# Performance work log

Measured on AMD Instinct MI355X. Metric: run time of the kernel, lower is better.

Reference implementation:

```python
import jax, jax.numpy as jnp
import numpy as np

D_MODEL = 1024
NUM_HEADS = 16
HEAD_DIM = D_MODEL // NUM_HEADS  # 64
ROPE_THETA = 10000.0
SEQ_LEN = 4096
BATCH = 1


def apply_rope(x, positions, theta=ROPE_THETA):
    # x: [b, h, s, d], positions: [s]
    d = x.shape[-1]
    inv_freq = theta ** (-jnp.arange(0, d, 2, dtype=jnp.float32) / d)  # [d/2]
    angles = positions.astype(jnp.float32)[:, None] * inv_freq[None, :]  # [s, d/2]
    cos = jnp.cos(angles)  # [s, d/2]
    sin = jnp.sin(angles)
    x1 = x[..., 0::2]  # [b, h, s, d/2]
    x2 = x[..., 1::2]
    r1 = x1 * cos - x2 * sin
    r2 = x1 * sin + x2 * cos
    # interleave back to [..., d]
    out = jnp.stack([r1, r2], axis=-1).reshape(x.shape)
    return out.astype(x.dtype)


def setup_inputs() -> dict:
    key = jax.random.key(0)
    k_x, k_qkv, k_o = jax.random.split(key, 3)
    scale_in = 1.0 / np.sqrt(D_MODEL)
    return {
        "x": jax.random.normal(k_x, (BATCH, SEQ_LEN, D_MODEL), dtype=jnp.float32),
        "token_positions": jnp.arange(SEQ_LEN, dtype=jnp.int64 if jax.config.jax_enable_x64 else jnp.int32),
        "w_qkv": jax.random.normal(k_qkv, (3 * D_MODEL, D_MODEL), dtype=jnp.float32) * scale_in,
        "w_o": jax.random.normal(k_o, (D_MODEL, D_MODEL), dtype=jnp.float32) * scale_in,
    }


def reference(x, token_positions, w_qkv, w_o):
    b, s, _ = x.shape
    # QKV projection (Linear without bias, weight [out, in])
    x_qkv = jnp.einsum('bsd,ed->bse', x, w_qkv)  # [b, s, 3*d_model]
    # rearrange 'b s (three heads kv) -> three b heads s kv'
    x_qkv = x_qkv.reshape(b, s, 3, NUM_HEADS, HEAD_DIM)
    x_qkv = jnp.transpose(x_qkv, (2, 0, 3, 1, 4))  # [3, b, h, s, d]
    q, k, v = x_qkv[0], x_qkv[1], x_qkv[2]
    q = apply_rope(q, token_positions)
    k = apply_rope(k, token_positions)
    # scaled dot-product attention with causal mask
    scores = jnp.einsum('bhnd,bhmd->bhnm', q, k) / jnp.sqrt(jnp.float32(HEAD_DIM))
    causal = jnp.tril(jnp.ones((s, s), dtype=bool))  # [s, s]
    scores = jnp.where(causal[None, None], scores, jnp.float32(-jnp.inf))
    weights = jax.nn.softmax(scores, axis=-1)
    attn = jnp.einsum('bhnm,bhmd->bhnd', weights, v)  # [b, h, s, d]
    attn = jnp.transpose(attn, (0, 2, 1, 3)).reshape(b, s, NUM_HEADS * HEAD_DIM)
    return jnp.einsum('bsd,ed->bse', attn, w_o)
```

## Files before the change

### kernel.cpp

```cpp
#include <hip/hip_runtime.h>

#define SEQ 4096
#define DMODEL 1024
#define HEADS 16
#define HD 64
#define NQKV 3072

typedef __attribute__((ext_vector_type(8))) __bf16 bf16x8;
typedef __attribute__((ext_vector_type(4))) __bf16 bf16x4;
typedef __attribute__((ext_vector_type(8))) short short8;
typedef __attribute__((ext_vector_type(4))) float f32x4;
typedef __attribute__((ext_vector_type(16))) float f32x16;
typedef __attribute__((ext_vector_type(4))) unsigned int u32x4;

__device__ __forceinline__ unsigned short f2bf(float f) {
    unsigned u = __builtin_bit_cast(unsigned, f);
    return (unsigned short)((u + 0x7fffu + ((u >> 16) & 1u)) >> 16);
}
__device__ __forceinline__ float bf2f(unsigned short h) {
    return __builtin_bit_cast(float, (unsigned)h << 16);
}
__device__ __forceinline__ unsigned cvt_pk_bf16(float lo, float hi) {
    unsigned r;
    asm("v_cvt_pk_bf16_f32 %0, %1, %2" : "=v"(r) : "v"(lo), "v"(hi));
    return r;
}

__device__ __forceinline__ void gload16(const void* g, void* l) {
    __builtin_amdgcn_global_load_lds(
        (const __attribute__((address_space(1))) unsigned int*)g,
        (__attribute__((address_space(3))) unsigned int*)l, 16, 0, 0);
}

#define TS(qt, kh) (0x40 | ((kh) << 5) | (qt))
__device__ __constant__ unsigned char TASKS[28] = {
    TS(15,0), TS(15,1), TS(14,0), TS(14,1), TS(13,0), TS(13,1),
    TS(12,0), TS(12,1), TS(11,0), TS(11,1), TS(10,0), TS(10,1),
    TS(9,0),  TS(9,1),  TS(8,0),  TS(8,1),  TS(7,0),  TS(7,1),
    3,        TS(6,0),  TS(6,1),  2,        TS(5,0),  TS(5,1),
    TS(4,0),  TS(4,1),  1,        0
};

__global__ void f2bf_all(const float* __restrict__ x, const float* __restrict__ wqkv,
                         const float* __restrict__ wo, const int* __restrict__ pos,
                         unsigned short* __restrict__ dst,
                         float* __restrict__ csT, float* __restrict__ snT) {
    const int N0 = SEQ * DMODEL / 4;
    const int N1 = N0 + NQKV * DMODEL / 4;
    const int NT = N1 + DMODEL * DMODEL / 4;
    int i = blockIdx.x * 256 + threadIdx.x;
    int stride = gridDim.x * 256;
    for (; i < NT; i += stride) {
        const float4* src;
        if (i < N0)      src = reinterpret_cast<const float4*>(x) + i;
        else if (i < N1) src = reinterpret_cast<const float4*>(wqkv) + (i - N0);
        else             src = reinterpret_cast<const float4*>(wo) + (i - N1);
        float4 f = *src;
        ushort4 o;
        o.x = f2bf(f.x); o.y = f2bf(f.y); o.z = f2bf(f.z); o.w = f2bf(f.w);
        reinterpret_cast<ushort4*>(dst)[i] = o;
    }
    const float kk = -13.287712379549449f / 32.0f;
    for (int idx = blockIdx.x * 256 + threadIdx.x; idx < SEQ * 32; idx += stride) {
        int s = idx >> 5, fi = idx & 31;
        float p = (float)pos[s];
        float ang = p * exp2f((float)fi * kk);
        float sn_, cs_;
        sincosf(ang, &sn_, &cs_);
        csT[idx] = cs_;
        snT[idx] = sn_;
    }
}

template <int EPI>
__global__ __launch_bounds__(256) void gemm_bt(const unsigned short* __restrict__ A,
                                               const unsigned short* __restrict__ B,
                                               float* __restrict__ outF,
                                               unsigned short* __restrict__ outB,
                                               unsigned short* __restrict__ vtp,
                                               const float* __restrict__ csT,
                                               const float* __restrict__ snT,
                                               int M, int N, int K) {
    alignas(16) __shared__ unsigned short a_lds[2][128 * 32];
    alignas(16) __shared__ unsigned short b_lds[2][128 * 32];
    __shared__ unsigned short vtile[4][16][72];
    const int tid = threadIdx.x;
    const int wave = tid >> 6, lane = tid & 63;
    const int l16 = lane & 15, g = lane >> 4;
    const int wr = wave >> 1, wc = wave & 1;
    const int bm = blockIdx.x, bn = blockIdx.y;

    const int lrow = lane >> 2;
    const int lcol = (lane & 3) * 8;

    const unsigned short* Ag = A + (size_t)(bm * 128 + lrow) * K + lcol;
    const unsigned short* Bg = B + (size_t)(bn * 128 + lrow) * K + lcol;

    f32x4 acc[4][4] = {};
    const int NS = K / 32;

    auto STAGE = [&](int b, int ks) {
#pragma unroll
        for (int j = 0; j < 2; ++j) {
            int chunk = wave * 2 + j;
            gload16(Ag + (size_t)(chunk * 16) * K + ks * 32, a_lds[b] + chunk * 512);
            gload16(Bg + (size_t)(chunk * 16) * K + ks * 32, b_lds[b] + chunk * 512);
        }
    };

    STAGE(0, 0);

    for (int ks = 0; ks < NS; ++ks) {
        const int cur = ks & 1;
        asm volatile("s_waitcnt vmcnt(0)" ::: "memory");
        __builtin_amdgcn_s_barrier();
        if (ks + 1 < NS) STAGE(cur ^ 1, ks + 1);

        bf16x8 af[4], bfr[4];
#pragma unroll
        for (int m = 0; m < 4; ++m)
            af[m] = *reinterpret_cast<const bf16x8*>(a_lds[cur] + (wr * 64 + m * 16 + l16) * 32 + g * 8);
#pragma unroll
        for (int n = 0; n < 4; ++n)
            bfr[n] = *reinterpret_cast<const bf16x8*>(b_lds[cur] + (wc * 64 + n * 16 + l16) * 32 + g * 8);
        __builtin_amdgcn_s_setprio(1);
#pragma unroll
        for (int m = 0; m < 4; ++m)
#pragma unroll
            for (int n = 0; n < 4; ++n)
                acc[m][n] = __builtin_amdgcn_mfma_f32_16x16x32_bf16(af[m], bfr[n], acc[m][n], 0, 0, 0);
        __builtin_amdgcn_s_setprio(0);
    }

    if (EPI == 0) {
        const float QS = 0.125f * 1.4426950408889634f;
#pragma unroll
        for (int n = 0; n < 4; ++n) {
            const int col = bn * 128 + wc * 64 + n * 16 + l16;
            const int part = col >> 10;
            const int hh = (col >> 6) & 15;
            const int d = n * 16 + l16;
            if (part < 2) {
                const int fi = (col & 63) >> 1;
                const float sc = (part == 0) ? QS : 1.0f;
                const bool odd = (col & 1) != 0;
#pragma unroll
                for (int m = 0; m < 4; ++m)
#pragma unroll
                    for (int r = 0; r < 4; ++r) {
                        int row = bm * 128 + wr * 64 + m * 16 + g * 4 + r;
                        float v = acc[m][n][r];
                        float pp = __shfl_xor(v, 1);
                        float cs_ = csT[row * 32 + fi];
                        float sn_ = snT[row * 32 + fi];
                        float out = odd ? (pp * sn_ + v * cs_) : (v * cs_ - pp * sn_);
                        outB[(size_t)((part * HEADS + hh) * SEQ + row) * HD + (col & 63)] = f2bf(out * sc);
                    }
            } else {
#pragma unroll
                for (int m = 0; m < 4; ++m)
#pragma unroll
                    for (int r = 0; r < 4; ++r)
                        vtile[wave][l16][m * 16 + g * 4 + r] = f2bf(acc[m][n][r]);
#pragma unroll
                for (int dd = 0; dd < 16; ++dd) {
                    int dg = ((col & 63) & ~15) + dd;
                    vtp[(size_t)(hh * HD + dg) * SEQ + bm * 128 + wr * 64 + lane] =
                        vtile[wave][dd][lane];
                }
            }
        }
    } else {
#pragma unroll
        for (int m = 0; m < 4; ++m)
#pragma unroll
            for (int n = 0; n < 4; ++n)
#pragma unroll
                for (int r = 0; r < 4; ++r) {
                    int row = bm * 128 + wr * 64 + m * 16 + g * 4 + r;
                    int col = bn * 128 + wc * 64 + n * 16 + l16;
                    outF[(size_t)row * N + col] = acc[m][n][r];
                }
    }
}

__global__ __launch_bounds__(512) void attn_kernel(const unsigned short* __restrict__ qkv,
                                                   const unsigned short* __restrict__ vt,
                                                   unsigned short* __restrict__ attnout,
                                                   int* __restrict__ qcnt,
                                                   unsigned short* __restrict__ pO,
                                                   float* __restrict__ lmf) {
    const int xcd = blockIdx.x & 7;
    const int tid = threadIdx.x;
    const int wave = tid >> 6, lane = tid & 63;
    const int l32 = lane & 31, hi = lane >> 5;

    alignas(16) __shared__ unsigned short k_lds[2][128 * 64];
    alignas(16) __shared__ unsigned short v_lds[2][2][64 * 64];
    __shared__ int slot_sh;

    const int rsw = (l32 & 7) << 4;

    for (;;) {
        if (tid == 0) slot_sh = atomicAdd(&qcnt[xcd], 1);
        __syncthreads();
        const int t = slot_sh;
        __syncthreads();
        if (t >= 56) break;

        const int hloc = t & 1;
        const unsigned char e = TASKS[t >> 1];
        const int qtile = e & 31;
        const int khalf = (e >> 5) & 1;
        const bool isSplit = (e >> 6) != 0;
        const int T = 2 * qtile + 2, Hh = qtile + 1;
        const int k0 = isSplit ? (khalf ? Hh : 0) : 0;
        const int k1 = isSplit ? (khalf ? T : Hh) : T;
        const int h = xcd * 2 + hloc;

        const unsigned short* Qg = qkv + (size_t)((0 * HEADS + h) * SEQ) * HD;
        const unsigned short* Kg = qkv + (size_t)((1 * HEADS + h) * SEQ) * HD;
        const unsigned short* VTg = vt + (size_t)h * HD * SEQ;

        const int qbase = qtile * 256 + wave * 32;
        const int qrow = qbase + l32;

        bf16x8 qf[4];
#pragma unroll
        for (int dg = 0; dg < 4; ++dg)
            qf[dg] = *reinterpret_cast<const bf16x8*>(Qg + (size_t)qrow * HD + dg * 16 + hi * 8);

        f32x16 oa[2] = {};
        float m_r = -1e30f, l_r = 0.f;

        auto STAGE = [&](int b, int kt) {
#pragma unroll
            for (int i = 0; i < 2; ++i) {
                int base = wave * 2048 + i * 1024;
                int byte = base + lane * 16;
                int krow = byte >> 7;
                int kc8 = ((byte >> 4) & 7) ^ (krow & 7);
                gload16(Kg + (size_t)(kt * 128 + krow) * HD + kc8 * 8, (char*)k_lds[b] + base);
                int fr = byte >> 7;
                int h64 = fr >> 6, vd = fr & 63;
                int vc8 = ((byte >> 4) & 7) ^ (vd & 7);
                gload16(VTg + (size_t)vd * SEQ + kt * 128 + h64 * 64 + vc8 * 8,
                        (char*)v_lds[b] + base);
            }
        };

        STAGE(0, k0);

        for (int kt = k0; kt < k1; ++kt) {
            const int cur = (kt - k0) & 1;
            asm volatile("s_waitcnt vmcnt(0)" ::: "memory");
            __builtin_amdgcn_s_barrier();
            if (kt + 1 < k1) STAGE(cur ^ 1, kt + 1);

#pragma unroll
            for (int hh = 0; hh < 2; ++hh) {
                if (hh && (kt * 128 + 64) > (qbase + 31)) break;

                f32x16 s[2] = {};
                __builtin_amdgcn_s_setprio(1);
#pragma unroll
                for (int g = 0; g < 2; ++g) {
                    int row = hh * 64 + g * 32 + l32;
#pragma unroll
                    for (int dg = 0; dg < 4; ++dg) {
                        bf16x8 kf = *reinterpret_cast<const bf16x8*>(
                            (char*)k_lds[cur] + row * 128 + ((dg * 32 + hi * 16) ^ rsw));
                        s[g] = __builtin_amdgcn_mfma_f32_32x32x16_bf16(kf, qf[dg], s[g], 0, 0, 0);
                    }
                }
                __builtin_amdgcn_s_setprio(0);

                if (kt * 128 + hh * 64 + 63 > qbase) {
#pragma unroll
                    for (int g = 0; g < 2; ++g)
#pragma unroll
                        for (int r = 0; r < 16; ++r) {
                            int kv = kt * 128 + hh * 64 + g * 32 + (r & 3) + 8 * (r >> 2) + 4 * hi;
                            if (kv > qrow) s[g][r] = -1e30f;
                        }
                }

                float ma = -1e30f, mb = -1e30f, mc = -1e30f, md = -1e30f;
#pragma unroll
                for (int r = 0; r < 16; r += 4) {
                    ma = fmaxf(ma, fmaxf(s[0][r], s[1][r]));
                    mb = fmaxf(mb, fmaxf(s[0][r + 1], s[1][r + 1]));
                    mc = fmaxf(mc, fmaxf(s[0][r + 2], s[1][r + 2]));
                    md = fmaxf(md, fmaxf(s[0][r + 3], s[1][r + 3]));
                }
                float mx = fmaxf(fmaxf(ma, mb), fmaxf(mc, md));
                mx = fmaxf(mx, __shfl_xor(mx, 32));

                if (__any(mx > m_r + 8.0f)) {
                    float mnew = fmaxf(m_r, mx);
                    float alpha = __builtin_amdgcn_exp2f(m_r - mnew);
                    m_r = mnew;
#pragma unroll
                    for (int r = 0; r < 16; ++r) { oa[0][r] *= alpha; oa[1][r] *= alpha; }
                    l_r *= alpha;
                }

#pragma unroll
                for (int g = 0; g < 2; ++g)
#pragma unroll
                    for (int r = 0; r < 16; ++r) s[g][r] = __builtin_amdgcn_exp2f(s[g][r] - m_r);

                float ra = 0.f, rb = 0.f;
#pragma unroll
                for (int r = 0; r < 16; r += 2) {
                    ra += s[0][r] + s[1][r];
                    rb += s[0][r + 1] + s[1][r + 1];
                }
                float rs = ra + rb;
                rs += __shfl_xor(rs, 32);
                l_r += rs;

                __builtin_amdgcn_s_setprio(1);
#pragma unroll
                for (int g = 0; g < 2; ++g) {
                    u32x4 pfw[2];
#pragma unroll
                    for (int u = 0; u < 2; ++u) {
                        unsigned wA = cvt_pk_bf16(s[g][8 * u + 0], s[g][8 * u + 1]);
                        unsigned wC = cvt_pk_bf16(s[g][8 * u + 2], s[g][8 * u + 3]);
                        unsigned wB = cvt_pk_bf16(s[g][8 * u + 4], s[g][8 * u + 5]);
                        unsigned wD = cvt_pk_bf16(s[g][8 * u + 6], s[g][8 * u + 7]);
                        unsigned wAx = __shfl_xor((int)wA, 32), wBx = __shfl_xor((int)wB, 32);
                        unsigned wCx = __shfl_xor((int)wC, 32), wDx = __shfl_xor((int)wD, 32);
                        pfw[u][0] = hi ? wBx : wA;
                        pfw[u][1] = hi ? wDx : wC;
                        pfw[u][2] = hi ? wB : wAx;
                        pfw[u][3] = hi ? wD : wCx;
                    }
#pragma unroll
                    for (int u = 0; u < 2; ++u) {
                        bf16x8 pf = __builtin_bit_cast(bf16x8, pfw[u]);
                        int ks = g * 2 + u;
#pragma unroll
                        for (int dg = 0; dg < 2; ++dg) {
                            bf16x8 vf = *reinterpret_cast<const bf16x8*>(
                                (char*)v_lds[cur][hh] + (dg * 32 + l32) * 128 + ((ks * 32 + hi * 16) ^ rsw));
                            oa[dg] = __builtin_amdgcn_mfma_f32_32x32x16_bf16(vf, pf, oa[dg], 0, 0, 0);
                        }
                    }
                }
                __builtin_amdgcn_s_setprio(0);
            }
        }

        const int ql = wave * 32 + l32;
        if (isSplit) {
            int sidx = (h * 12 + (qtile - 4)) * 2 + khalf;
            unsigned short* Op = pO + (size_t)sidx * 16384;
#pragma unroll
            for (int dg = 0; dg < 2; ++dg)
#pragma unroll
                for (int rq = 0; rq < 4; ++rq) {
                    ushort4 ov;
                    ov.x = f2bf(oa[dg][4 * rq + 0]);
                    ov.y = f2bf(oa[dg][4 * rq + 1]);
                    ov.z = f2bf(oa[dg][4 * rq + 2]);
                    ov.w = f2bf(oa[dg][4 * rq + 3]);
                    *reinterpret_cast<ushort4*>(Op + ql * 64 + dg * 32 + 8 * rq + 4 * hi) = ov;
                }
            if (hi == 0) {
                lmf[sidx * 512 + ql] = l_r;
                lmf[sidx * 512 + 256 + ql] = m_r;
            }
        } else {
            float inv = 1.0f / l_r;
            unsigned short* orow = attnout + (size_t)(qtile * 256 + ql) * DMODEL + h * HD;
#pragma unroll
            for (int dg = 0; dg < 2; ++dg)
#pragma unroll
                for (int rq = 0; rq < 4; ++rq) {
                    ushort4 ov;
                    ov.x = f2bf(oa[dg][4 * rq + 0] * inv);
                    ov.y = f2bf(oa[dg][4 * rq + 1] * inv);
                    ov.z = f2bf(oa[dg][4 * rq + 2] * inv);
                    ov.w = f2bf(oa[dg][4 * rq + 3] * inv);
                    *reinterpret_cast<ushort4*>(orow + dg * 32 + 8 * rq + 4 * hi) = ov;
                }
        }
    }
}

__global__ __launch_bounds__(256) void merge_kernel(const unsigned short* __restrict__ pO,
                                                    const float* __restrict__ lmf,
                                                    unsigned short* __restrict__ attnout) {
    int idx = blockIdx.x * 256 + threadIdx.x;
    if (idx >= 16 * 12 * 2048) return;
    int h = idx / (12 * 2048);
    int r = idx % (12 * 2048);
    int qt = r >> 11;
    int rr = r & 2047;
    int q = rr >> 3, d8 = rr & 7;

    int s0 = (h * 12 + qt) * 2;
    float l0 = lmf[s0 * 512 + q],       m0 = lmf[s0 * 512 + 256 + q];
    float l1 = lmf[(s0 + 1) * 512 + q], m1 = lmf[(s0 + 1) * 512 + 256 + q];
    float m = fmaxf(m0, m1);
    float a0 = __builtin_amdgcn_exp2f(m0 - m), a1 = __builtin_amdgcn_exp2f(m1 - m);
    float L = l0 * a0 + l1 * a1;
    float c0 = a0 / L, c1 = a1 / L;

    const unsigned short* O0 = pO + (size_t)s0 * 16384 + q * 64 + d8 * 8;
    const unsigned short* O1 = O0 + 16384;
    short8 v0 = *reinterpret_cast<const short8*>(O0);
    short8 v1 = *reinterpret_cast<const short8*>(O1);
    short8 o;
#pragma unroll
    for (int j = 0; j < 8; ++j) {
        float val = bf2f((unsigned short)v0[j]) * c0 + bf2f((unsigned short)v1[j]) * c1;
        o[j] = (short)f2bf(val);
    }
    int qtile = qt + 4;
    *reinterpret_cast<short8*>(attnout + (size_t)(qtile * 256 + q) * DMODEL + h * HD + d8 * 8) = o;
}

extern "C" void kernel_launch(void* const* d_in, const int* in_sizes, int n_in,
                              void* d_out, int out_size, void* d_ws, size_t ws_size,
                              hipStream_t stream) {
    const float* x = (const float*)d_in[0];
    const int* pos = (const int*)d_in[1];
    const float* wqkv = (const float*)d_in[2];
    const float* wo = (const float*)d_in[3];
    float* out = (float*)d_out;

    unsigned short* xb = (unsigned short*)d_ws;
    unsigned short* wqkvb = xb + (size_t)SEQ * DMODEL;
    unsigned short* wob = wqkvb + (size_t)NQKV * DMODEL;
    unsigned short* qkvp = wob + (size_t)DMODEL * DMODEL;
    unsigned short* vtp = qkvp + (size_t)2 * HEADS * SEQ * HD;
    float* csT = (float*)(qkvp + (size_t)3 * HEADS * SEQ * HD);
    float* snT = csT + SEQ * 32;
    unsigned short* attnb = (unsigned short*)(snT + SEQ * 32);

    char* sbase = (char*)d_ws;
    int* qcnt = (int*)sbase;
    float* lmf = (float*)(sbase + 1024);
    unsigned short* pO = (unsigned short*)(sbase + (1 << 20));

    f2bf_all<<<2048, 256, 0, stream>>>(x, wqkv, wo, pos, xb, csT, snT);

    dim3 g1(SEQ / 128, NQKV / 128);
    gemm_bt<0><<<g1, 256, 0, stream>>>(xb, wqkvb, nullptr, qkvp, vtp, csT, snT, SEQ, NQKV, DMODEL);

    hipMemsetAsync(qcnt, 0, 64, stream);
    attn_kernel<<<512, 512, 0, stream>>>(qkvp, vtp, attnb, qcnt, pO, lmf);
    merge_kernel<<<(16 * 12 * 2048 + 255) / 256, 256, 0, stream>>>(pO, lmf, attnb);

    dim3 g2(SEQ / 128, DMODEL / 128);
    gemm_bt<1><<<g2, 256, 0, stream>>>(attnb, wob, out, nullptr, nullptr, nullptr, nullptr, SEQ, DMODEL, DMODEL);
}
```

Measured before the change: 137.6 us.

## Split GEMM into QKV and output kernels with XCD-aware remap and narrower tiles

Splits the templated GEMM into two kernels. The QKV projection now uses a 1D grid whose block index is remapped so blocks sharing an XCD (bid & 7) get contiguous tiles, aiming at better L2 reuse of A and B panels. The output projection switches to 128x64 tiles, doubling the block count to 512 so more CUs stay busy on the small 4096x1024 GEMM. The smaller tile costs arithmetic intensity, since each B-tile load now feeds half as many MFMAs.

```diff
diff --git a/kernel.cpp b/kernel.cpp
--- a/kernel.cpp
+++ b/kernel.cpp
@@ -72,15 +72,13 @@
     }
 }
 
-template <int EPI>
-__global__ __launch_bounds__(256) void gemm_bt(const unsigned short* __restrict__ A,
-                                               const unsigned short* __restrict__ B,
-                                               float* __restrict__ outF,
-                                               unsigned short* __restrict__ outB,
-                                               unsigned short* __restrict__ vtp,
-                                               const float* __restrict__ csT,
-                                               const float* __restrict__ snT,
-                                               int M, int N, int K) {
+__global__ __launch_bounds__(256) void gemm_qkv(const unsigned short* __restrict__ A,
+                                                const unsigned short* __restrict__ B,
+                                                unsigned short* __restrict__ outB,
+                                                unsigned short* __restrict__ vtp,
+                                                const float* __restrict__ csT,
+                                                const float* __restrict__ snT,
+                                                int M, int N, int K) {
     alignas(16) __shared__ unsigned short a_lds[2][128 * 32];
     alignas(16) __shared__ unsigned short b_lds[2][128 * 32];
     __shared__ unsigned short vtile[4][16][72];
@@ -88,7 +86,10 @@
     const int wave = tid >> 6, lane = tid & 63;
     const int l16 = lane & 15, g = lane >> 4;
     const int wr = wave >> 1, wc = wave & 1;
-    const int bm = blockIdx.x, bn = blockIdx.y;
+
+    const int bid = blockIdx.x;
+    const int t = (bid & 7) * 96 + (bid >> 3);
+    const int bm = t / 24, bn = t % 24;
 
     const int lrow = lane >> 2;
     const int lcol = (lane & 3) * 8;
@@ -132,56 +133,108 @@
         __builtin_amdgcn_s_setprio(0);
     }
 
-    if (EPI == 0) {
-        const float QS = 0.125f * 1.4426950408889634f;
-#pragma unroll
-        for (int n = 0; n < 4; ++n) {
-            const int col = bn * 128 + wc * 64 + n * 16 + l16;
-            const int part = col >> 10;
-            const int hh = (col >> 6) & 15;
-            const int d = n * 16 + l16;
-            if (part < 2) {
-                const int fi = (col & 63) >> 1;
-                const float sc = (part == 0) ? QS : 1.0f;
-                const bool odd = (col & 1) != 0;
-#pragma unroll
-                for (int m = 0; m < 4; ++m)
-#pragma unroll
-                    for (int r = 0; r < 4; ++r) {
-                        int row = bm * 128 + wr * 64 + m * 16 + g * 4 + r;
-                        float v = acc[m][n][r];
-                        float pp = __shfl_xor(v, 1);
-                        float cs_ = csT[row * 32 + fi];
-                        float sn_ = snT[row * 32 + fi];
-                        float out = odd ? (pp * sn_ + v * cs_) : (v * cs_ - pp * sn_);
-                        outB[(size_t)((part * HEADS + hh) * SEQ + row) * HD + (col & 63)] = f2bf(out * sc);
-                    }
-            } else {
-#pragma unroll
-                for (int m = 0; m < 4; ++m)
-#pragma unroll
-                    for (int r = 0; r < 4; ++r)
-                        vtile[wave][l16][m * 16 + g * 4 + r] = f2bf(acc[m][n][r]);
-#pragma unroll
-                for (int dd = 0; dd < 16; ++dd) {
-                    int dg = ((col & 63) & ~15) + dd;
-                    vtp[(size_t)(hh * HD + dg) * SEQ + bm * 128 + wr * 64 + lane] =
-                        vtile[wave][dd][lane];
-                }
+    const float QS = 0.125f * 1.4426950408889634f;
+#pragma unroll
+    for (int n = 0; n < 4; ++n) {
+        const int col = bn * 128 + wc * 64 + n * 16 + l16;
+        const int part = col >> 10;
+        const int hh = (col >> 6) & 15;
+        if (part < 2) {
+            const int fi = (col & 63) >> 1;
+            const float sc = (part == 0) ? QS : 1.0f;
+            const bool odd = (col & 1) != 0;
+#pragma unroll
+            for (int m = 0; m < 4; ++m)
+#pragma unroll
+                for (int r = 0; r < 4; ++r) {
+                    int row = bm * 128 + wr * 64 + m * 16 + g * 4 + r;
+                    float v = acc[m][n][r];
+                    float pp = __shfl_xor(v, 1);
+                    float cs_ = csT[row * 32 + fi];
+                    float sn_ = snT[row * 32 + fi];
+                    float out = odd ? (pp * sn_ + v * cs_) : (v * cs_ - pp * sn_);
+                    outB[(size_t)((part * HEADS + hh) * SEQ + row) * HD + (col & 63)] = f2bf(out * sc);
+                }
+        } else {
+#pragma unroll
+            for (int m = 0; m < 4; ++m)
+#pragma unroll
+                for (int r = 0; r < 4; ++r)
+                    vtile[wave][l16][m * 16 + g * 4 + r] = f2bf(acc[m][n][r]);
+#pragma unroll
+            for (int dd = 0; dd < 16; ++dd) {
+                int dg = ((col & 63) & ~15) + dd;
+                vtp[(size_t)(hh * HD + dg) * SEQ + bm * 128 + wr * 64 + lane] =
+                    vtile[wave][dd][lane];
             }
         }
-    } else {
+    }
+}
+
+__global__ __launch_bounds__(256) void gemm_out(const unsigned short* __restrict__ A,
+                                                const unsigned short* __restrict__ B,
+                                                float* __restrict__ outF,
+                                                int M, int N, int K) {
+    alignas(16) __shared__ unsigned short a_lds[2][128 * 32];
+    alignas(16) __shared__ unsigned short b_lds[2][64 * 32];
+    const int tid = threadIdx.x;
+    const int wave = tid >> 6, lane = tid & 63;
+    const int l16 = lane & 15, g = lane >> 4;
+    const int wr = wave >> 1, wc = wave & 1;
+    const int bm = blockIdx.x, bn = blockIdx.y;
+
+    const int lrow = lane >> 2;
+    const int lcol = (lane & 3) * 8;
+
+    const unsigned short* Ag = A + (size_t)(bm * 128 + lrow) * K + lcol;
+    const unsigned short* Bg = B + (size_t)(bn * 64 + lrow) * K + lcol;
+
+    f32x4 acc[4][2] = {};
+    const int NS = K / 32;
+
+    auto STAGE = [&](int b, int ks) {
+#pragma unroll
+        for (int j = 0; j < 2; ++j) {
+            int chunk = wave * 2 + j;
+            gload16(Ag + (size_t)(chunk * 16) * K + ks * 32, a_lds[b] + chunk * 512);
+        }
+        gload16(Bg + (size_t)(wave * 16) * K + ks * 32, b_lds[b] + wave * 512);
+    };
+
+    STAGE(0, 0);
+
+    for (int ks = 0; ks < NS; ++ks) {
+        const int cur = ks & 1;
+        asm volatile("s_waitcnt vmcnt(0)" ::: "memory");
+        __builtin_amdgcn_s_barrier();
+        if (ks + 1 < NS) STAGE(cur ^ 1, ks + 1);
+
+        bf16x8 af[4], bfr[2];
 #pragma unroll
         for (int m = 0; m < 4; ++m)
-#pragma unroll
-            for (int n = 0; n < 4; ++n)
-#pragma unroll
-                for (int r = 0; r < 4; ++r) {
-                    int row = bm * 128 + wr * 64 + m * 16 + g * 4 + r;
-                    int col = bn * 128 + wc * 64 + n * 16 + l16;
-                    outF[(size_t)row * N + col] = acc[m][n][r];
-                }
-    }
+            af[m] = *reinterpret_cast<const bf16x8*>(a_lds[cur] + (wr * 64 + m * 16 + l16) * 32 + g * 8);
+#pragma unroll
+        for (int n = 0; n < 2; ++n)
+            bfr[n] = *reinterpret_cast<const bf16x8*>(b_lds[cur] + (wc * 32 + n * 16 + l16) * 32 + g * 8);
+        __builtin_amdgcn_s_setprio(1);
+#pragma unroll
+        for (int m = 0; m < 4; ++m)
+#pragma unroll
+            for (int n = 0; n < 2; ++n)
+                acc[m][n] = __builtin_amdgcn_mfma_f32_16x16x32_bf16(af[m], bfr[n], acc[m][n], 0, 0, 0);
+        __builtin_amdgcn_s_setprio(0);
+    }
+
+#pragma unroll
+    for (int m = 0; m < 4; ++m)
+#pragma unroll
+        for (int n = 0; n < 2; ++n)
+#pragma unroll
+            for (int r = 0; r < 4; ++r) {
+                int row = bm * 128 + wr * 64 + m * 16 + g * 4 + r;
+                int col = bn * 64 + wc * 32 + n * 16 + l16;
+                outF[(size_t)row * N + col] = acc[m][n][r];
+            }
 }
 
 __global__ __launch_bounds__(512) void attn_kernel(const unsigned short* __restrict__ qkv,
@@ -448,13 +501,12 @@
 
     f2bf_all<<<2048, 256, 0, stream>>>(x, wqkv, wo, pos, xb, csT, snT);
 
-    dim3 g1(SEQ / 128, NQKV / 128);
-    gemm_bt<0><<<g1, 256, 0, stream>>>(xb, wqkvb, nullptr, qkvp, vtp, csT, snT, SEQ, NQKV, DMODEL);
+    gemm_qkv<<<768, 256, 0, stream>>>(xb, wqkvb, qkvp, vtp, csT, snT, SEQ, NQKV, DMODEL);
 
     hipMemsetAsync(qcnt, 0, 64, stream);
     attn_kernel<<<512, 512, 0, stream>>>(qkvp, vtp, attnb, qcnt, pO, lmf);
     merge_kernel<<<(16 * 12 * 2048 + 255) / 256, 256, 0, stream>>>(pO, lmf, attnb);
 
-    dim3 g2(SEQ / 128, DMODEL / 128);
-    gemm_bt<1><<<g2, 256, 0, stream>>>(attnb, wob, out, nullptr, nullptr, nullptr, nullptr, SEQ, DMODEL, DMODEL);
-}
+    dim3 g2(SEQ / 128, DMODEL / 64);
+    gemm_out<<<g2, 256, 0, stream>>>(attnb, wob, out, SEQ, DMODEL, DMODEL);
+}
```

Result: no change. 137.1 us (-0.4%).
